# Kernel tuning notes

Hardware: AMD Instinct MI355X
Metric: run time of the kernel (lower is better)

The kernel has to match this reference:

```python
import jax, jax.numpy as jnp
import numpy as np

NODELEN = 17949
N_NODES = 512
N_EDGES = 4096
H2 = 768
EMB = 128
IN_DIM = 2 * NODELEN


def _seg_mean(h, src, dst, n):
    # gather neighbor features and mean-reduce per destination node
    msg = h[src]                                   # [E, F]
    s = jax.ops.segment_sum(msg, dst, num_segments=n)
    deg = jax.ops.segment_sum(jnp.ones((src.shape[0],), h.dtype), dst, num_segments=n)
    return s / jnp.maximum(deg, 1.0)[:, None]


def setup_inputs() -> dict:
    key = jax.random.key(0)
    ks = jax.random.split(key, 12)
    s = 0.02
    return {
        "x": jax.random.normal(ks[0], (N_NODES, NODELEN), jnp.float32),
        "edge_src": jax.random.randint(ks[1], (N_EDGES,), 0, N_NODES),
        "edge_dst": jax.random.randint(ks[2], (N_EDGES,), 0, N_NODES),
        "W_e2": jax.random.normal(ks[3], (H2, IN_DIM), jnp.float32) * s,
        "b_e2": jnp.zeros((H2,), jnp.float32),
        "W_e3": jax.random.normal(ks[4], (EMB, H2), jnp.float32) * s,
        "b_e3": jnp.zeros((EMB,), jnp.float32),
        "W_d1": jax.random.normal(ks[5], (H2, EMB), jnp.float32) * s,
        "b_d1": jnp.zeros((H2,), jnp.float32),
        "W_d3": jax.random.normal(ks[6], (IN_DIM, H2), jnp.float32) * s,
        "b_d3": jnp.zeros((IN_DIM,), jnp.float32),
    }


def reference(x, edge_src, edge_dst, W_e2, b_e2, W_e3, b_e3, W_d1, b_d1, W_d3, b_d3):
    n = x.shape[0]
    # depth-2 recursive GraphSAGE mean aggregation; agg[0]=0 after each hop
    h1 = _seg_mean(x, edge_src, edge_dst, n).at[:, 0].set(0.0)
    h2 = _seg_mean(h1, edge_src, edge_dst, n).at[:, 0].set(0.0)
    emb = jnp.concatenate([x, h2], axis=1)           # [N, 2*NODELEN]
    emb = emb.at[:, 0].set(0.0).at[:, NODELEN].set(0.0)
    # AutoEncoder (eval mode: dropout is identity)
    h = jax.nn.relu(emb @ W_e2.T + b_e2)
    encoded = h @ W_e3.T + b_e3
    h = jax.nn.relu(encoded @ W_d1.T + b_d1)
    decoded = h @ W_d3.T + b_d3
    return encoded, decoded
```

## Files before the change

kernel.cpp:

```cpp
#include <hip/hip_runtime.h>
#include <hip/hip_bf16.h>

#define NODELEN 17949
#define NN 512
#define NE 4096
#define H2 768
#define EMB 128
#define IN_DIM (2 * NODELEN)
#define KP1 35904
#define KITERS1 561
#define SPLITS 24
#define KCHUNK1 24

#define BM 128
#define BN 128
#define BK 64
#define LDT (BK + 8)

typedef __bf16 bf16x8 __attribute__((ext_vector_type(8)));
typedef float f32x4 __attribute__((ext_vector_type(4)));


__global__ void k_zero_int(int* p, int n) {
    int i = blockIdx.x * 256 + threadIdx.x;
    if (i < n) p[i] = 0;
}

__global__ void k_zero_f4(float4* p, int n4) {
    int i = blockIdx.x * 256 + threadIdx.x;
    if (i < n4) p[i] = make_float4(0.f, 0.f, 0.f, 0.f);
}

__global__ void k_deg(const int* __restrict__ dst, int* __restrict__ cnt) {
    int e = blockIdx.x * 256 + threadIdx.x;
    if (e < NE) atomicAdd(&cnt[dst[e]], 1);
}

__global__ void k_invdeg(const int* __restrict__ cnt, float* __restrict__ invdeg) {
    int i = blockIdx.x * 256 + threadIdx.x;
    if (i < NN) {
        int c = cnt[i];
        invdeg[i] = 1.0f / (float)(c > 1 ? c : 1);
    }
}

__global__ void k_scatter(const int* __restrict__ src, const int* __restrict__ dst,
                          const float* __restrict__ invdeg, float* __restrict__ A) {
    int e = blockIdx.x * 256 + threadIdx.x;
    if (e < NE) {
        int d = dst[e];
        atomicAdd(&A[(size_t)d * NN + src[e]], invdeg[d]);
    }
}

__global__ void k_a2(const float* __restrict__ A, __bf16* __restrict__ A2b) {
    int i = blockIdx.x;
    int t = threadIdx.x;
    __shared__ float row[NN];
    row[t] = A[(size_t)i * NN + t];
    row[t + 256] = A[(size_t)i * NN + 256 + t];
    __syncthreads();
    float a0 = 0.f, a1 = 0.f;
    for (int s = 0; s < NN; ++s) {
        float a = row[s];
        if (a != 0.f) {
            a0 += a * A[(size_t)s * NN + t];
            a1 += a * A[(size_t)s * NN + 256 + t];
        }
    }
    A2b[(size_t)i * NN + t] = (__bf16)a0;
    A2b[(size_t)i * NN + 256 + t] = (__bf16)a1;
}

__global__ void k_xt(const float* __restrict__ x, __bf16* __restrict__ xT) {
    __shared__ float t[64][65];
    int f0 = blockIdx.x * 64, s0 = blockIdx.y * 64;
    int tx = threadIdx.x & 63, ty = threadIdx.x >> 6;
#pragma unroll
    for (int r = 0; r < 16; ++r) {
        int f = f0 + tx;
        t[ty * 16 + r][tx] = (f < NODELEN) ? x[(size_t)(s0 + ty * 16 + r) * NODELEN + f] : 0.f;
    }
    __syncthreads();
#pragma unroll
    for (int r = 0; r < 16; ++r) {
        int f = f0 + ty * 16 + r;
        if (f < NODELEN) xT[(size_t)f * NN + s0 + tx] = (__bf16)t[tx][ty * 16 + r];
    }
}

__global__ void k_embx(const float* __restrict__ x, __bf16* __restrict__ embb) {
    int c = blockIdx.x * 256 + threadIdx.x;
    int n = blockIdx.y;
    if (c < NODELEN) {
        float v = (c == 0) ? 0.f : x[(size_t)n * NODELEN + c];
        embb[(size_t)n * KP1 + c] = (__bf16)v;
    } else {
        int cc = c - NODELEN;
        if (cc < KP1 - IN_DIM) embb[(size_t)n * KP1 + IN_DIM + cc] = (__bf16)0.f;
    }
}

__global__ void k_cvt_we2(const float* __restrict__ W, __bf16* __restrict__ Wb) {
    const int C8 = KP1 / 8;
    int idx = blockIdx.x * 256 + threadIdx.x;
    if (idx >= H2 * C8) return;
    int r = idx / C8, c8 = (idx % C8) * 8;
    __align__(16) __bf16 o[8];
    if (c8 + 8 <= IN_DIM) {
        const float2* p = (const float2*)(W + (size_t)r * IN_DIM + c8);
#pragma unroll
        for (int j = 0; j < 4; ++j) {
            float2 f = p[j];
            o[2 * j] = (__bf16)f.x;
            o[2 * j + 1] = (__bf16)f.y;
        }
    } else {
#pragma unroll
        for (int j = 0; j < 8; ++j) {
            int c = c8 + j;
            o[j] = (c < IN_DIM) ? (__bf16)W[(size_t)r * IN_DIM + c] : (__bf16)0.f;
        }
    }
    *(uint4*)&Wb[(size_t)r * KP1 + c8] = *(uint4*)o;
}


template <int EPI, bool BF16B>
__global__ __launch_bounds__(256) void gemm_k(
        const __bf16* __restrict__ A, int lda,
        const void* __restrict__ Bv, int ldb,
        int Nvalid, int kIters, int kChunk,
        float* __restrict__ Cf, int ldc, const float* __restrict__ bias,
        __bf16* __restrict__ Cb) {
    __shared__ __align__(16) __bf16 As[BM][LDT];
    __shared__ __align__(16) __bf16 Bs[BN][LDT];

    const int tid = threadIdx.x;
    const int m0 = blockIdx.x * BM;
    const int n0 = blockIdx.y * BN;
    const int z = blockIdx.z;

    int it0 = z * kChunk;
    int it1 = it0 + kChunk;
    if (it1 > kIters) it1 = kIters;

    const int wave = tid >> 6;
    const int lane = tid & 63;
    const int wm = (wave & 1) * 64;
    const int wn = (wave >> 1) * 64;
    const int fl = lane & 15;
    const int fq = lane >> 4;

    const int srow = tid >> 1;
    const int spart = tid & 1;

    f32x4 acc[4][4] = {};

    const int bn = n0 + srow;
    const bool nok = bn < Nvalid;

    for (int it = it0; it < it1; ++it) {
        int k0 = it * BK;

        {
            const uint4* Ag = (const uint4*)(A + (size_t)(m0 + srow) * lda + k0 + spart * 32);
            uint4 av[4];
#pragma unroll
            for (int i = 0; i < 4; ++i) av[i] = Ag[i];
#pragma unroll
            for (int i = 0; i < 4; ++i)
                *(uint4*)&As[srow][spart * 32 + i * 8] = av[i];
        }
        if (BF16B) {
            uint4 bv[4];
            if (nok) {
                const uint4* Bg = (const uint4*)((const __bf16*)Bv + (size_t)bn * ldb + k0 + spart * 32);
#pragma unroll
                for (int i = 0; i < 4; ++i) bv[i] = Bg[i];
            } else {
#pragma unroll
                for (int i = 0; i < 4; ++i) bv[i] = make_uint4(0, 0, 0, 0);
            }
#pragma unroll
            for (int i = 0; i < 4; ++i)
                *(uint4*)&Bs[srow][spart * 32 + i * 8] = bv[i];
        } else {
            __align__(16) __bf16 bl[32];
            if (nok) {
                const float4* Bg = (const float4*)((const float*)Bv + (size_t)bn * ldb + k0 + spart * 32);
                float4 f[8];
#pragma unroll
                for (int j = 0; j < 8; ++j) f[j] = Bg[j];
#pragma unroll
                for (int j = 0; j < 8; ++j) {
                    bl[4 * j] = (__bf16)f[j].x;
                    bl[4 * j + 1] = (__bf16)f[j].y;
                    bl[4 * j + 2] = (__bf16)f[j].z;
                    bl[4 * j + 3] = (__bf16)f[j].w;
                }
            } else {
#pragma unroll
                for (int j = 0; j < 32; ++j) bl[j] = (__bf16)0.f;
            }
#pragma unroll
            for (int q = 0; q < 4; ++q)
                *(uint4*)&Bs[srow][spart * 32 + q * 8] = *(uint4*)&bl[q * 8];
        }
        __syncthreads();

#pragma unroll
        for (int ks = 0; ks < 2; ++ks) {
            int kk = ks * 32 + fq * 8;
            bf16x8 af[4], bf[4];
#pragma unroll
            for (int i = 0; i < 4; ++i)
                af[i] = *(const bf16x8*)&As[wm + i * 16 + fl][kk];
#pragma unroll
            for (int j = 0; j < 4; ++j)
                bf[j] = *(const bf16x8*)&Bs[wn + j * 16 + fl][kk];
#pragma unroll
            for (int i = 0; i < 4; ++i)
#pragma unroll
                for (int j = 0; j < 4; ++j)
                    acc[i][j] = __builtin_amdgcn_mfma_f32_16x16x32_bf16(
                        af[i], bf[j], acc[i][j], 0, 0, 0);
        }
        __syncthreads();
    }

#pragma unroll
    for (int i = 0; i < 4; ++i) {
#pragma unroll
        for (int j = 0; j < 4; ++j) {
#pragma unroll
            for (int r = 0; r < 4; ++r) {
                int m = m0 + wm + i * 16 + fq * 4 + r;
                int n = n0 + wn + j * 16 + fl;
                float v = acc[i][j][r];
                if (EPI == 0) {
                    Cf[((size_t)z * NN + m) * H2 + n] = v;
                } else if (EPI == 1) {
                    if (n < Nvalid) Cf[(size_t)m * ldc + n] = v + bias[n];
                } else {
                    if (n < Nvalid)
                        Cb[(size_t)m * KP1 + NODELEN + n] = (n == 0) ? (__bf16)0.f : (__bf16)v;
                }
            }
        }
    }
}

__global__ void k_reduce(const float* __restrict__ partials,
                         const float* __restrict__ bias, float* __restrict__ h) {
    int idx = blockIdx.x * 256 + threadIdx.x;
    if (idx >= NN * H2) return;
    float s = 0.f;
#pragma unroll
    for (int zz = 0; zz < SPLITS; ++zz) s += partials[(size_t)zz * NN * H2 + idx];
    s += bias[idx % H2];
    h[idx] = s > 0.f ? s : 0.f;
}

__global__ void k_enc(const float* __restrict__ h, const float* __restrict__ W,
                      const float* __restrict__ b, float* __restrict__ out) {
    int m = blockIdx.x, e = threadIdx.x;
    const float4* hr = (const float4*)(h + (size_t)m * H2);
    const float4* wr = (const float4*)(W + (size_t)e * H2);
    float s = 0.f;
#pragma unroll 4
    for (int i = 0; i < H2 / 4; ++i) {
        float4 a = hr[i];
        float4 w = wr[i];
        s += a.x * w.x + a.y * w.y + a.z * w.z + a.w * w.w;
    }
    out[(size_t)m * EMB + e] = s + b[e];
}

__global__ void k_dec1(const float* __restrict__ enc, const float* __restrict__ W,
                       const float* __restrict__ b, __bf16* __restrict__ hd) {
    int m = blockIdx.x;
    __shared__ float er[EMB];
    if (threadIdx.x < EMB) er[threadIdx.x] = enc[(size_t)m * EMB + threadIdx.x];
    __syncthreads();
    for (int j = threadIdx.x; j < H2; j += 256) {
        const float4* wr = (const float4*)(W + (size_t)j * EMB);
        float s = 0.f;
#pragma unroll
        for (int i = 0; i < EMB / 4; ++i) {
            float4 w = wr[i];
            s += w.x * er[4 * i] + w.y * er[4 * i + 1] + w.z * er[4 * i + 2] +
                 w.w * er[4 * i + 3];
        }
        float v = s + b[j];
        hd[(size_t)m * H2 + j] = (__bf16)(v > 0.f ? v : 0.f);
    }
}


extern "C" void kernel_launch(void* const* d_in, const int* in_sizes, int n_in,
                              void* d_out, int out_size, void* d_ws, size_t ws_size,
                              hipStream_t stream) {
    const float* x = (const float*)d_in[0];
    const int* esrc = (const int*)d_in[1];
    const int* edst = (const int*)d_in[2];
    const float* W_e2 = (const float*)d_in[3];
    const float* b_e2 = (const float*)d_in[4];
    const float* W_e3 = (const float*)d_in[5];
    const float* b_e3 = (const float*)d_in[6];
    const float* W_d1 = (const float*)d_in[7];
    const float* b_d1 = (const float*)d_in[8];
    const float* W_d3 = (const float*)d_in[9];
    const float* b_d3 = (const float*)d_in[10];
    float* out = (float*)d_out;

    char* w = (char*)d_ws;
    auto alloc = [&](size_t bytes) {
        char* p = w;
        w += (bytes + 255) & ~(size_t)255;
        return p;
    };
    __bf16* embb = (__bf16*)alloc((size_t)NN * KP1 * 2);
    __bf16* We2b = (__bf16*)alloc((size_t)H2 * KP1 * 2);
    char* uni = (char*)alloc((size_t)SPLITS * NN * H2 * 4);
    __bf16* xTb = (__bf16*)uni;
    float* Adj = (float*)(uni + (size_t)17952 * NN * 2);
    __bf16* A2b = (__bf16*)((char*)Adj + (size_t)NN * NN * 4);
    int* cnt = (int*)((char*)A2b + (size_t)NN * NN * 2);
    float* invdeg = (float*)((char*)cnt + 2048);
    float* partials = (float*)uni;
    float* h = (float*)alloc((size_t)NN * H2 * 4);
    __bf16* hd_b = (__bf16*)alloc((size_t)NN * H2 * 2);

    k_zero_int<<<2, 256, 0, stream>>>(cnt, NN);
    k_zero_f4<<<256, 256, 0, stream>>>((float4*)Adj, NN * NN / 4);
    k_deg<<<NE / 256, 256, 0, stream>>>(edst, cnt);
    k_invdeg<<<2, 256, 0, stream>>>(cnt, invdeg);
    k_scatter<<<NE / 256, 256, 0, stream>>>(esrc, edst, invdeg, Adj);
    k_a2<<<NN, 256, 0, stream>>>(Adj, A2b);

    dim3 gxt((NODELEN + 63) / 64, NN / 64);
    k_xt<<<gxt, 256, 0, stream>>>(x, xTb);
    dim3 gex((NODELEN + 255) / 256, NN);
    k_embx<<<gex, 256, 0, stream>>>(x, embb);

    dim3 gh2(NN / BM, (NODELEN + BN - 1) / BN, 1);
    gemm_k<2, true><<<gh2, 256, 0, stream>>>(
        A2b, NN, xTb, NN, NODELEN, NN / BK, NN / BK,
        (float*)nullptr, 0, (const float*)nullptr, embb);

    k_cvt_we2<<<(H2 * (KP1 / 8) + 255) / 256, 256, 0, stream>>>(W_e2, We2b);

    dim3 g1(NN / BM, H2 / BN, SPLITS);
    gemm_k<0, true><<<g1, 256, 0, stream>>>(
        embb, KP1, We2b, KP1, H2, KITERS1, KCHUNK1,
        partials, 0, (const float*)nullptr, (__bf16*)nullptr);

    k_reduce<<<(NN * H2) / 256, 256, 0, stream>>>(partials, b_e2, h);

    k_enc<<<NN, EMB, 0, stream>>>(h, W_e3, b_e3, out);

    k_dec1<<<NN, 256, 0, stream>>>(out, W_d1, b_d1, hd_b);

    dim3 g4(NN / BM, (IN_DIM + BN - 1) / BN, 1);
    gemm_k<1, false><<<g4, 256, 0, stream>>>(
        hd_b, H2, W_d3, H2, IN_DIM, H2 / BK, H2 / BK,
        out + (size_t)NN * EMB, IN_DIM, b_d3, (__bf16*)nullptr);
}
```

Measured before the change: 592.3 us.

## Fuse fp32 W_e2 conversion into GEMM, merge x transpose/emb, prefetch, XCD remap

```diff
diff --git a/kernel.cpp b/kernel.cpp
--- a/kernel.cpp
+++ b/kernel.cpp
@@ -72,14 +72,19 @@
     A2b[(size_t)i * NN + 256 + t] = (__bf16)a1;
 }
 
-__global__ void k_xt(const float* __restrict__ x, __bf16* __restrict__ xT) {
+__global__ void k_xt_emb(const float* __restrict__ x, __bf16* __restrict__ xT,
+                         __bf16* __restrict__ embb) {
     __shared__ float t[64][65];
     int f0 = blockIdx.x * 64, s0 = blockIdx.y * 64;
     int tx = threadIdx.x & 63, ty = threadIdx.x >> 6;
 #pragma unroll
     for (int r = 0; r < 16; ++r) {
         int f = f0 + tx;
-        t[ty * 16 + r][tx] = (f < NODELEN) ? x[(size_t)(s0 + ty * 16 + r) * NODELEN + f] : 0.f;
+        int s = s0 + ty * 16 + r;
+        float v = (f < NODELEN) ? x[(size_t)s * NODELEN + f] : 0.f;
+        t[ty * 16 + r][tx] = v;
+        if (f < NODELEN)
+            embb[(size_t)s * KP1 + f] = (__bf16)((f == 0) ? 0.f : v);
     }
     __syncthreads();
 #pragma unroll
@@ -89,57 +94,73 @@
     }
 }
 
-__global__ void k_embx(const float* __restrict__ x, __bf16* __restrict__ embb) {
-    int c = blockIdx.x * 256 + threadIdx.x;
-    int n = blockIdx.y;
-    if (c < NODELEN) {
-        float v = (c == 0) ? 0.f : x[(size_t)n * NODELEN + c];
-        embb[(size_t)n * KP1 + c] = (__bf16)v;
-    } else {
-        int cc = c - NODELEN;
-        if (cc < KP1 - IN_DIM) embb[(size_t)n * KP1 + IN_DIM + cc] = (__bf16)0.f;
-    }
-}
-
-__global__ void k_cvt_we2(const float* __restrict__ W, __bf16* __restrict__ Wb) {
-    const int C8 = KP1 / 8;
-    int idx = blockIdx.x * 256 + threadIdx.x;
-    if (idx >= H2 * C8) return;
-    int r = idx / C8, c8 = (idx % C8) * 8;
-    __align__(16) __bf16 o[8];
-    if (c8 + 8 <= IN_DIM) {
-        const float2* p = (const float2*)(W + (size_t)r * IN_DIM + c8);
-#pragma unroll
-        for (int j = 0; j < 4; ++j) {
-            float2 f = p[j];
-            o[2 * j] = (__bf16)f.x;
-            o[2 * j + 1] = (__bf16)f.y;
-        }
-    } else {
-#pragma unroll
-        for (int j = 0; j < 8; ++j) {
-            int c = c8 + j;
-            o[j] = (c < IN_DIM) ? (__bf16)W[(size_t)r * IN_DIM + c] : (__bf16)0.f;
-        }
-    }
-    *(uint4*)&Wb[(size_t)r * KP1 + c8] = *(uint4*)o;
-}
-
+__global__ void k_pad(__bf16* __restrict__ embb) {
+    int i = blockIdx.x * 256 + threadIdx.x;
+    const int PAD = KP1 - IN_DIM;
+    if (i < NN * PAD) {
+        int n = i / PAD, c = i % PAD;
+        embb[(size_t)n * KP1 + IN_DIM + c] = (__bf16)0.f;
+    }
+}
+
+
+#define GLOAD(K0)                                                                    \
+    do {                                                                             \
+        const uint4* Ag_ = (const uint4*)(Arow + (K0));                              \
+        _Pragma("unroll")                                                            \
+        for (int i_ = 0; i_ < 4; ++i_) av[i_] = Ag_[i_];                             \
+        if (BF16B) {                                                                 \
+            if (nok) {                                                               \
+                const uint4* Bg_ = (const uint4*)(Brow_h + (K0));                    \
+                _Pragma("unroll")                                                    \
+                for (int i_ = 0; i_ < 4; ++i_) bvh[i_] = Bg_[i_];                    \
+            } else {                                                                 \
+                _Pragma("unroll")                                                    \
+                for (int i_ = 0; i_ < 4; ++i_) bvh[i_] = make_uint4(0, 0, 0, 0);     \
+            }                                                                        \
+        } else {                                                                     \
+            if (nok && ((K0) + spart * 32 + 32 <= Kvalid)) {                         \
+                const float4* Bg_ = (const float4*)(Brow_f + (K0));                  \
+                _Pragma("unroll")                                                    \
+                for (int j_ = 0; j_ < 8; ++j_) bvf[j_] = Bg_[j_];                    \
+            } else {                                                                 \
+                _Pragma("unroll")                                                    \
+                for (int j_ = 0; j_ < 8; ++j_) {                                     \
+                    int kb_ = (K0) + spart * 32 + j_ * 4;                            \
+                    float4 v_;                                                       \
+                    v_.x = (nok && kb_ + 0 < Kvalid) ? Brow_f[(K0) + j_ * 4 + 0] : 0.f; \
+                    v_.y = (nok && kb_ + 1 < Kvalid) ? Brow_f[(K0) + j_ * 4 + 1] : 0.f; \
+                    v_.z = (nok && kb_ + 2 < Kvalid) ? Brow_f[(K0) + j_ * 4 + 2] : 0.f; \
+                    v_.w = (nok && kb_ + 3 < Kvalid) ? Brow_f[(K0) + j_ * 4 + 3] : 0.f; \
+                    bvf[j_] = v_;                                                    \
+                }                                                                    \
+            }                                                                        \
+        }                                                                            \
+    } while (0)
 
 template <int EPI, bool BF16B>
 __global__ __launch_bounds__(256) void gemm_k(
         const __bf16* __restrict__ A, int lda,
         const void* __restrict__ Bv, int ldb,
-        int Nvalid, int kIters, int kChunk,
+        int Nvalid, int Kvalid, int kIters, int kChunk,
         float* __restrict__ Cf, int ldc, const float* __restrict__ bias,
         __bf16* __restrict__ Cb) {
     __shared__ __align__(16) __bf16 As[BM][LDT];
     __shared__ __align__(16) __bf16 Bs[BN][LDT];
 
     const int tid = threadIdx.x;
-    const int m0 = blockIdx.x * BM;
-    const int n0 = blockIdx.y * BN;
-    const int z = blockIdx.z;
+
+    const int gx = gridDim.x, gy = gridDim.y;
+    const int nwg = gx * gy * (int)gridDim.z;
+    const int fid = blockIdx.x + gx * (blockIdx.y + gy * blockIdx.z);
+    const int q = nwg >> 3, r = nwg & 7;
+    const int xcd = fid & 7, idx = fid >> 3;
+    const int lid = (xcd < r) ? xcd * (q + 1) + idx
+                              : r * (q + 1) + (xcd - r) * q + idx;
+    const int m0 = (lid % gx) * BM;
+    const int rem = lid / gx;
+    const int n0 = (rem % gy) * BN;
+    const int z = rem / gy;
 
     int it0 = z * kChunk;
     int it1 = it0 + kChunk;
@@ -159,55 +180,40 @@
 
     const int bn = n0 + srow;
     const bool nok = bn < Nvalid;
+    const __bf16* Arow = A + (size_t)(m0 + srow) * lda + spart * 32;
+    const __bf16* Brow_h = (const __bf16*)Bv + (size_t)bn * ldb + spart * 32;
+    const float* Brow_f = (const float*)Bv + (size_t)bn * ldb + spart * 32;
+
+    uint4 av[4];
+    uint4 bvh[4];
+    float4 bvf[8];
+
+    if (it0 < it1) GLOAD(it0 * BK);
 
     for (int it = it0; it < it1; ++it) {
-        int k0 = it * BK;
-
-        {
-            const uint4* Ag = (const uint4*)(A + (size_t)(m0 + srow) * lda + k0 + spart * 32);
-            uint4 av[4];
-#pragma unroll
-            for (int i = 0; i < 4; ++i) av[i] = Ag[i];
+#pragma unroll
+        for (int i = 0; i < 4; ++i)
+            *(uint4*)&As[srow][spart * 32 + i * 8] = av[i];
+        if (BF16B) {
 #pragma unroll
             for (int i = 0; i < 4; ++i)
-                *(uint4*)&As[srow][spart * 32 + i * 8] = av[i];
-        }
-        if (BF16B) {
-            uint4 bv[4];
-            if (nok) {
-                const uint4* Bg = (const uint4*)((const __bf16*)Bv + (size_t)bn * ldb + k0 + spart * 32);
-#pragma unroll
-                for (int i = 0; i < 4; ++i) bv[i] = Bg[i];
-            } else {
-#pragma unroll
-                for (int i = 0; i < 4; ++i) bv[i] = make_uint4(0, 0, 0, 0);
-            }
-#pragma unroll
-            for (int i = 0; i < 4; ++i)
-                *(uint4*)&Bs[srow][spart * 32 + i * 8] = bv[i];
+                *(uint4*)&Bs[srow][spart * 32 + i * 8] = bvh[i];
         } else {
             __align__(16) __bf16 bl[32];
-            if (nok) {
-                const float4* Bg = (const float4*)((const float*)Bv + (size_t)bn * ldb + k0 + spart * 32);
-                float4 f[8];
-#pragma unroll
-                for (int j = 0; j < 8; ++j) f[j] = Bg[j];
-#pragma unroll
-                for (int j = 0; j < 8; ++j) {
-                    bl[4 * j] = (__bf16)f[j].x;
-                    bl[4 * j + 1] = (__bf16)f[j].y;
-                    bl[4 * j + 2] = (__bf16)f[j].z;
-                    bl[4 * j + 3] = (__bf16)f[j].w;
-                }
-            } else {
-#pragma unroll
-                for (int j = 0; j < 32; ++j) bl[j] = (__bf16)0.f;
+#pragma unroll
+            for (int j = 0; j < 8; ++j) {
+                bl[4 * j + 0] = (__bf16)bvf[j].x;
+                bl[4 * j + 1] = (__bf16)bvf[j].y;
+                bl[4 * j + 2] = (__bf16)bvf[j].z;
+                bl[4 * j + 3] = (__bf16)bvf[j].w;
             }
 #pragma unroll
-            for (int q = 0; q < 4; ++q)
-                *(uint4*)&Bs[srow][spart * 32 + q * 8] = *(uint4*)&bl[q * 8];
+            for (int qq = 0; qq < 4; ++qq)
+                *(uint4*)&Bs[srow][spart * 32 + qq * 8] = *(uint4*)&bl[qq * 8];
         }
         __syncthreads();
+
+        if (it + 1 < it1) GLOAD((it + 1) * BK);
 
 #pragma unroll
         for (int ks = 0; ks < 2; ++ks) {
@@ -234,10 +240,10 @@
 #pragma unroll
         for (int j = 0; j < 4; ++j) {
 #pragma unroll
-            for (int r = 0; r < 4; ++r) {
-                int m = m0 + wm + i * 16 + fq * 4 + r;
+            for (int rr = 0; rr < 4; ++rr) {
+                int m = m0 + wm + i * 16 + fq * 4 + rr;
                 int n = n0 + wn + j * 16 + fl;
-                float v = acc[i][j][r];
+                float v = acc[i][j][rr];
                 if (EPI == 0) {
                     Cf[((size_t)z * NN + m) * H2 + n] = v;
                 } else if (EPI == 1) {
@@ -321,7 +327,6 @@
         return p;
     };
     __bf16* embb = (__bf16*)alloc((size_t)NN * KP1 * 2);
-    __bf16* We2b = (__bf16*)alloc((size_t)H2 * KP1 * 2);
     char* uni = (char*)alloc((size_t)SPLITS * NN * H2 * 4);
     __bf16* xTb = (__bf16*)uni;
     float* Adj = (float*)(uni + (size_t)17952 * NN * 2);
@@ -340,20 +345,17 @@
     k_a2<<<NN, 256, 0, stream>>>(Adj, A2b);
 
     dim3 gxt((NODELEN + 63) / 64, NN / 64);
-    k_xt<<<gxt, 256, 0, stream>>>(x, xTb);
-    dim3 gex((NODELEN + 255) / 256, NN);
-    k_embx<<<gex, 256, 0, stream>>>(x, embb);
+    k_xt_emb<<<gxt, 256, 0, stream>>>(x, xTb, embb);
+    k_pad<<<(NN * (KP1 - IN_DIM) + 255) / 256, 256, 0, stream>>>(embb);
 
     dim3 gh2(NN / BM, (NODELEN + BN - 1) / BN, 1);
     gemm_k<2, true><<<gh2, 256, 0, stream>>>(
-        A2b, NN, xTb, NN, NODELEN, NN / BK, NN / BK,
+        A2b, NN, xTb, NN, NODELEN, NN, NN / BK, NN / BK,
         (float*)nullptr, 0, (const float*)nullptr, embb);
 
-    k_cvt_we2<<<(H2 * (KP1 / 8) + 255) / 256, 256, 0, stream>>>(W_e2, We2b);
-
     dim3 g1(NN / BM, H2 / BN, SPLITS);
-    gemm_k<0, true><<<g1, 256, 0, stream>>>(
-        embb, KP1, We2b, KP1, H2, KITERS1, KCHUNK1,
+    gemm_k<0, false><<<g1, 256, 0, stream>>>(
+        embb, KP1, W_e2, IN_DIM, H2, IN_DIM, KITERS1, KCHUNK1,
         partials, 0, (const float*)nullptr, (__bf16*)nullptr);
 
     k_reduce<<<(NN * H2) / 256, 256, 0, stream>>>(partials, b_e2, h);
@@ -364,6 +366,6 @@
 
     dim3 g4(NN / BM, (IN_DIM + BN - 1) / BN, 1);
     gemm_k<1, false><<<g4, 256, 0, stream>>>(
-        hd_b, H2, W_d3, H2, IN_DIM, H2 / BK, H2 / BK,
+        hd_b, H2, W_d3, H2, IN_DIM, H2, H2 / BK, H2 / BK,
         out + (size_t)NN * EMB, IN_DIM, b_d3, (__bf16*)nullptr);
 }
```

Result: slower. 782.3 us (+32.1%).
